# Optimization experiments

Measured on AMD Instinct MI355X. Metric: run time of the kernel, lower is better.

Reference implementation:

```python
import jax, jax.numpy as jnp
import numpy as np

EPS = 1e-7  # keras_backend.epsilon()
ROUTINGS = 3


def setup_inputs() -> dict:
    key = jax.random.key(0)
    k1, k2, k3, k4, k5 = jax.random.split(key, 5)
    B, H, W, I, O = 32, 8, 8, 32, 64
    return {
        "inputs_poses": jax.random.normal(k1, (B, H, W, I, 4, 4), dtype=jnp.float32),
        "inputs_activations": jax.random.uniform(k2, (B, H, W, I), dtype=jnp.float32),
        "w": jax.random.normal(k3, (I, O, 4, 4), dtype=jnp.float32),
        "beta_v": jax.random.normal(k4, (1, O), dtype=jnp.float32),
        "beta_a": jax.random.normal(k5, (1, O), dtype=jnp.float32),
    }


def _em_routing(votes, i_act, beta_v, beta_a, routings):
    # votes: [B, N, O, 16], i_act: [B, N]
    B, N, O, P = votes.shape
    act = i_act[..., None, None]              # [B, N, 1, 1]
    bv = beta_v[..., None, :, None]           # [1, 1, O, 1]
    ba = beta_a[..., None, :, None]           # [1, 1, O, 1]
    rr = jnp.full((N, O, 1), 1.0 / O, dtype=votes.dtype)
    it_min, it_max = 1.0, min(routings, 3.0)
    o_mean = o_act = None
    for it in range(routings):
        inv_temp = it_min + (it_max - it_min) * it / max(1.0, routings - 1.0)
        # ---- m-step ----
        rr_prime = rr * act                                    # [B, N, O, 1]
        rps = rr_prime.sum(axis=-3, keepdims=True)             # [B, 1, O, 1]
        o_mean = (rr_prime * votes).sum(axis=-3, keepdims=True) / rps   # [B,1,O,16]
        o_stdv = jnp.sqrt((rr_prime * jnp.square(votes - o_mean)).sum(axis=-3, keepdims=True) / rps)
        o_cost_h = (bv + jnp.log(o_stdv + EPS)) * rps          # [B,1,O,16]
        o_cost = o_cost_h.sum(axis=-1, keepdims=True)          # [B,1,O,1]
        o_cost_mean = o_cost.mean(axis=-2, keepdims=True)      # [B,1,1,1]
        o_cost_stdv = jnp.sqrt(jnp.square(o_cost - o_cost_mean).sum(axis=-2, keepdims=True) / O)
        o_act = jax.nn.sigmoid(inv_temp * (ba + (o_cost_mean - o_cost) / (o_cost_stdv + EPS)))
        # ---- e-step ----
        if it < routings - 1:
            o_p = (-jnp.sum(jnp.square(votes - o_mean) / (2.0 * jnp.square(o_stdv)), axis=-1, keepdims=True)
                   - jnp.sum(jnp.log(o_stdv + EPS), axis=-1, keepdims=True))   # [B,N,O,1]
            zz = jnp.log(o_act + EPS) + o_p
            rr = jax.nn.softmax(zz, axis=-2)                   # softmax over O
    poses = jnp.squeeze(o_mean, axis=-3)                       # [B, O, 16]
    activations = jnp.squeeze(o_act, axis=(-3, -1))            # [B, O]
    return poses, activations


def reference(inputs_poses, inputs_activations, w, beta_v, beta_a):
    B, H, W, I = inputs_activations.shape
    O = w.shape[1]
    # mat_transform: per-(input-type, class) 4x4 pose transform -> votes
    pose = inputs_poses.reshape(B * H * W, I, 4, 4)
    votes = jnp.einsum('siab,iobc->sioac', pose, w)            # [BHW, I, O, 4, 4]
    votes = votes.reshape(B, H, W, I, O, 16)
    # coord_addition: add scaled spatial coords to components 0 (h) and 1 (w)
    ch = jnp.zeros((1, H, 1, 1, 1, 16), votes.dtype).at[..., 0].set(
        ((jnp.arange(H, dtype=votes.dtype) + 0.5) / H).reshape(1, H, 1, 1, 1))
    cw = jnp.zeros((1, 1, W, 1, 1, 16), votes.dtype).at[..., 1].set(
        ((jnp.arange(W, dtype=votes.dtype) + 0.5) / W).reshape(1, 1, W, 1, 1))
    votes = votes + ch + cw
    votes = votes.reshape(B, H * W * I, O, 16)
    i_act = inputs_activations.reshape(B, H * W * I)
    poses, activations = _em_routing(votes, i_act, beta_v, beta_a, ROUTINGS)
    poses = poses.reshape(B, O, 4, 4)
    return poses, activations
```

## Files before the change

kernel.cpp:

```cpp
#include <hip/hip_runtime.h>


#define NB 32
#define NN 2048
#define NO 64
#define NP 16
#define EPSF 1e-7f

#define SITES_PB 8
#define IS_PB 16

#define ACC_SLOTS 33
#define ACC_PER_B (ACC_SLOTS * NO)
#define ACC_TOTAL (NB * ACC_PER_B)

template <bool FIRST>
__global__ __launch_bounds__(1024, 1) void accum_kernel(
    const float* __restrict__ pose,
    const float* __restrict__ act,
    const float* __restrict__ wmat,
    const float* __restrict__ beta_v,
    const float* __restrict__ beta_a,
    const float* __restrict__ accum_prev,
    float* __restrict__ accum_out,
    float inv_temp)
{
    __shared__ float stats_s[ACC_PER_B];
    __shared__ float buf[4][ACC_PER_B];

    const int b = blockIdx.y;
    const int sg = blockIdx.x >> 1;
    const int ig = blockIdx.x & 1;
    const int s0 = sg * SITES_PB;
    const int tid = threadIdx.x;
    const int w = tid >> 6;
    const int o = tid & 63;
    const int i = ig * 16 + w;
    const int grp = w >> 2, wvin = w & 3;

    const float4* wp = (const float4*)(wmat + ((size_t)i * 64 + o) * 16);
    float4 w0 = wp[0], w1 = wp[1], w2 = wp[2], w3 = wp[3];

    if (!FIRST && tid < 64) {
        const float* ap = accum_prev + (size_t)b * ACC_PER_B;
        float rps = ap[32 * 64 + o];
        float rinv = 1.0f / rps;
        float logsum = 0.f;
        float mm[16], vv[16];
        #pragma unroll
        for (int p = 0; p < 16; p++) {
            float mv = ap[p * 64 + o] * rinv;
            float va = fmaxf(ap[(16 + p) * 64 + o] * rinv - mv * mv, 0.f);
            mm[p] = mv;
            vv[p] = va;
            logsum += __logf(sqrtf(va) + EPSF);
        }
        float cost = rps * (16.0f * beta_v[o] + logsum);
        float cm = cost;
        #pragma unroll
        for (int s = 32; s > 0; s >>= 1) cm += __shfl_xor(cm, s, 64);
        cm *= (1.0f / 64.0f);
        float dd = cost - cm;
        float cs = dd * dd;
        #pragma unroll
        for (int s = 32; s > 0; s >>= 1) cs += __shfl_xor(cs, s, 64);
        cs = sqrtf(cs * (1.0f / 64.0f));
        float x = inv_temp * (beta_a[o] + (cm - cost) / (cs + EPSF));
        float oa = 1.0f / (1.0f + __expf(-x));
        float zzb = __logf(oa + EPSF) - logsum;
        float K = zzb;
        #pragma unroll
        for (int s = 32; s > 0; s >>= 1) K = fmaxf(K, __shfl_xor(K, s, 64));
        #pragma unroll
        for (int p = 0; p < 16; p++) stats_s[p * 64 + o] = mm[p];
        #pragma unroll
        for (int p = 0; p < 16; p++) stats_s[(16 + p) * 64 + o] = 0.5f / vv[p];
        stats_s[32 * 64 + o] = zzb - K;
    }
    __syncthreads();

    float m[16], i2v[16], zzbK = 0.f;
    if (!FIRST) {
        #pragma unroll
        for (int p = 0; p < 16; p++) m[p] = stats_s[p * 64 + o];
        #pragma unroll
        for (int p = 0; p < 16; p++) i2v[p] = stats_s[(16 + p) * 64 + o];
        zzbK = stats_s[32 * 64 + o];
    }

    float accR = 0.f, acc1[16], acc2[16];
    #pragma unroll
    for (int p = 0; p < 16; p++) { acc1[p] = 0.f; acc2[p] = 0.f; }

    const int base_n = __builtin_amdgcn_readfirstlane(s0 * 32 + ig * 16 + w);
    const float* pose_b = pose + (size_t)b * NN * 16;
    const float* act_b  = act + (size_t)b * NN;

    for (int sl = 0; sl < 8; sl++) {
        const int site = s0 + sl;
        const float c0 = ((site >> 3) + 0.5f) * 0.125f;
        const float c1 = ((site & 7) + 0.5f) * 0.125f;
        const int n = base_n + sl * 32;
        const float4* pr4 = (const float4*)(pose_b + (size_t)n * 16);
        const float av = act_b[n];

        float v[16];
        #pragma unroll
        for (int a = 0; a < 4; a++) {
            float4 pa = pr4[a];
            v[a * 4 + 0] = pa.x * w0.x + pa.y * w1.x + pa.z * w2.x + pa.w * w3.x;
            v[a * 4 + 1] = pa.x * w0.y + pa.y * w1.y + pa.z * w2.y + pa.w * w3.y;
            v[a * 4 + 2] = pa.x * w0.z + pa.y * w1.z + pa.z * w2.z + pa.w * w3.z;
            v[a * 4 + 3] = pa.x * w0.w + pa.y * w1.w + pa.z * w2.w + pa.w * w3.w;
        }
        v[0] += c0;
        v[1] += c1;

        float rr;
        if (FIRST) {
            rr = 1.0f / 64.0f;
        } else {
            float d = zzbK;
            #pragma unroll
            for (int p = 0; p < 16; p++) {
                float t = v[p] - m[p];
                d -= t * t * i2v[p];
            }
            float e = __expf(d);
            float sum = e;
            #pragma unroll
            for (int s = 32; s > 0; s >>= 1) sum += __shfl_xor(sum, s, 64);
            rr = e / fmaxf(sum, 1e-30f);
        }
        float rp = rr * av;
        accR += rp;
        #pragma unroll
        for (int p = 0; p < 16; p++) {
            acc1[p] += rp * v[p];
            acc2[p] += rp * v[p] * v[p];
        }
    }

    if (wvin == 3) {
        float* r = buf[grp];
        r[32 * 64 + o] = accR;
        #pragma unroll
        for (int p = 0; p < 16; p++) r[p * 64 + o] = acc1[p];
        #pragma unroll
        for (int p = 0; p < 16; p++) r[(16 + p) * 64 + o] = acc2[p];
    }
    __syncthreads();
    if (wvin == 2) {
        float* r = buf[grp];
        r[32 * 64 + o] += accR;
        #pragma unroll
        for (int p = 0; p < 16; p++) r[p * 64 + o] += acc1[p];
        #pragma unroll
        for (int p = 0; p < 16; p++) r[(16 + p) * 64 + o] += acc2[p];
    }
    __syncthreads();
    if (wvin == 1) {
        float* r = buf[grp];
        r[32 * 64 + o] += accR;
        #pragma unroll
        for (int p = 0; p < 16; p++) r[p * 64 + o] += acc1[p];
        #pragma unroll
        for (int p = 0; p < 16; p++) r[(16 + p) * 64 + o] += acc2[p];
    }
    __syncthreads();
    if (wvin == 0) {
        float* r = buf[grp];
        r[32 * 64 + o] += accR;
        #pragma unroll
        for (int p = 0; p < 16; p++) r[p * 64 + o] += acc1[p];
        #pragma unroll
        for (int p = 0; p < 16; p++) r[(16 + p) * 64 + o] += acc2[p];
    }
    __syncthreads();

    float* ac = accum_out + (size_t)b * ACC_PER_B;
    for (int j = tid; j < ACC_PER_B; j += 1024)
        atomicAdd(ac + j, buf[0][j] + buf[1][j] + buf[2][j] + buf[3][j]);
}

__global__ __launch_bounds__(64) void stats_final(
    const float* __restrict__ accum,
    const float* __restrict__ beta_v,
    const float* __restrict__ beta_a,
    float* __restrict__ out,
    float inv_temp)
{
    const int b = blockIdx.x;
    const int o = threadIdx.x;
    const float* ac = accum + (size_t)b * ACC_PER_B;

    float rps = ac[32 * 64 + o];
    float rinv = 1.0f / rps;
    float m[16];
    float logsum = 0.f;
    #pragma unroll
    for (int p = 0; p < 16; p++) {
        float mm = ac[p * 64 + o] * rinv;
        float vv = fmaxf(ac[(16 + p) * 64 + o] * rinv - mm * mm, 0.f);
        m[p] = mm;
        logsum += __logf(sqrtf(vv) + EPSF);
    }
    float cost = rps * (16.0f * beta_v[o] + logsum);

    float cm = cost;
    #pragma unroll
    for (int s = 32; s > 0; s >>= 1) cm += __shfl_xor(cm, s, 64);
    cm *= (1.0f / 64.0f);
    float dd = cost - cm;
    float cs = dd * dd;
    #pragma unroll
    for (int s = 32; s > 0; s >>= 1) cs += __shfl_xor(cs, s, 64);
    cs = sqrtf(cs * (1.0f / 64.0f));

    float x = inv_temp * (beta_a[o] + (cm - cost) / (cs + EPSF));
    float oa = 1.0f / (1.0f + __expf(-x));

    float* op = out + ((size_t)b * 64 + o) * 16;
    #pragma unroll
    for (int p = 0; p < 16; p++) op[p] = m[p];
    out[(size_t)NB * NO * NP + (size_t)b * 64 + o] = oa;
}

extern "C" void kernel_launch(void* const* d_in, const int* in_sizes, int n_in,
                              void* d_out, int out_size, void* d_ws, size_t ws_size,
                              hipStream_t stream) {
    const float* pose   = (const float*)d_in[0];
    const float* act    = (const float*)d_in[1];
    const float* wmat   = (const float*)d_in[2];
    const float* beta_v = (const float*)d_in[3];
    const float* beta_a = (const float*)d_in[4];
    float* out = (float*)d_out;
    float* ws = (float*)d_ws;

    float* a0 = ws;
    float* a1 = ws + (size_t)ACC_TOTAL;
    float* a2 = ws + 2 * (size_t)ACC_TOTAL;

    hipMemsetAsync(ws, 0, 3 * (size_t)ACC_TOTAL * sizeof(float), stream);

    dim3 grid(16, NB);
    accum_kernel<true ><<<grid, 1024, 0, stream>>>(pose, act, wmat, beta_v, beta_a,
                                                   nullptr, a0, 0.0f);
    accum_kernel<false><<<grid, 1024, 0, stream>>>(pose, act, wmat, beta_v, beta_a,
                                                   a0, a1, 1.0f);
    accum_kernel<false><<<grid, 1024, 0, stream>>>(pose, act, wmat, beta_v, beta_a,
                                                   a1, a2, 2.0f);
    stats_final<<<NB, 64, 0, stream>>>(a2, beta_v, beta_a, out, 3.0f);
}
```

Baseline: 146.5 us.

## Shrink accum blocks to four waves with longer site loops and register-level reduction

Each accumulation block now uses 256 threads covering 4 input types over 32 spatial sites, instead of 1024 threads covering 16 input types over 8 sites. The grid stays the same size, so each thread runs four times as many loop iterations. The cross-wave reduction becomes a two-level tree kept in registers, using half the shared buffer. Global atomics are issued straight from one wave's registers. This cuts reduction barriers, shared-memory traffic and prologue cost per unit of work, but leaves far fewer resident waves per CU, so memory and exp latency are harder to hide.

```diff
diff --git a/kernel.cpp b/kernel.cpp
--- a/kernel.cpp
+++ b/kernel.cpp
@@ -7,15 +7,12 @@
 #define NP 16
 #define EPSF 1e-7f
 
-#define SITES_PB 8
-#define IS_PB 16
-
 #define ACC_SLOTS 33
 #define ACC_PER_B (ACC_SLOTS * NO)
 #define ACC_TOTAL (NB * ACC_PER_B)
 
 template <bool FIRST>
-__global__ __launch_bounds__(1024, 1) void accum_kernel(
+__global__ __launch_bounds__(256, 2) void accum_kernel(
     const float* __restrict__ pose,
     const float* __restrict__ act,
     const float* __restrict__ wmat,
@@ -26,17 +23,16 @@
     float inv_temp)
 {
     __shared__ float stats_s[ACC_PER_B];
-    __shared__ float buf[4][ACC_PER_B];
+    __shared__ float red[2][ACC_PER_B];
 
     const int b = blockIdx.y;
-    const int sg = blockIdx.x >> 1;
-    const int ig = blockIdx.x & 1;
-    const int s0 = sg * SITES_PB;
+    const int sg = blockIdx.x >> 3;
+    const int ig = blockIdx.x & 7;
+    const int s0 = sg * 32;
     const int tid = threadIdx.x;
     const int w = tid >> 6;
     const int o = tid & 63;
-    const int i = ig * 16 + w;
-    const int grp = w >> 2, wvin = w & 3;
+    const int i = ig * 4 + w;
 
     const float4* wp = (const float4*)(wmat + ((size_t)i * 64 + o) * 16);
     float4 w0 = wp[0], w1 = wp[1], w2 = wp[2], w3 = wp[3];
@@ -92,11 +88,11 @@
     #pragma unroll
     for (int p = 0; p < 16; p++) { acc1[p] = 0.f; acc2[p] = 0.f; }
 
-    const int base_n = __builtin_amdgcn_readfirstlane(s0 * 32 + ig * 16 + w);
+    const int base_n = __builtin_amdgcn_readfirstlane(s0 * 32 + i);
     const float* pose_b = pose + (size_t)b * NN * 16;
     const float* act_b  = act + (size_t)b * NN;
 
-    for (int sl = 0; sl < 8; sl++) {
+    for (int sl = 0; sl < 32; sl++) {
         const int site = s0 + sl;
         const float c0 = ((site >> 3) + 0.5f) * 0.125f;
         const float c1 = ((site & 7) + 0.5f) * 0.125f;
@@ -141,8 +137,8 @@
         }
     }
 
-    if (wvin == 3) {
-        float* r = buf[grp];
+    if (w >= 2) {
+        float* r = red[w - 2];
         r[32 * 64 + o] = accR;
         #pragma unroll
         for (int p = 0; p < 16; p++) r[p * 64 + o] = acc1[p];
@@ -150,37 +146,39 @@
         for (int p = 0; p < 16; p++) r[(16 + p) * 64 + o] = acc2[p];
     }
     __syncthreads();
-    if (wvin == 2) {
-        float* r = buf[grp];
-        r[32 * 64 + o] += accR;
-        #pragma unroll
-        for (int p = 0; p < 16; p++) r[p * 64 + o] += acc1[p];
-        #pragma unroll
-        for (int p = 0; p < 16; p++) r[(16 + p) * 64 + o] += acc2[p];
-    }
-    __syncthreads();
-    if (wvin == 1) {
-        float* r = buf[grp];
-        r[32 * 64 + o] += accR;
-        #pragma unroll
-        for (int p = 0; p < 16; p++) r[p * 64 + o] += acc1[p];
-        #pragma unroll
-        for (int p = 0; p < 16; p++) r[(16 + p) * 64 + o] += acc2[p];
-    }
-    __syncthreads();
-    if (wvin == 0) {
-        float* r = buf[grp];
-        r[32 * 64 + o] += accR;
-        #pragma unroll
-        for (int p = 0; p < 16; p++) r[p * 64 + o] += acc1[p];
-        #pragma unroll
-        for (int p = 0; p < 16; p++) r[(16 + p) * 64 + o] += acc2[p];
-    }
-    __syncthreads();
-
-    float* ac = accum_out + (size_t)b * ACC_PER_B;
-    for (int j = tid; j < ACC_PER_B; j += 1024)
-        atomicAdd(ac + j, buf[0][j] + buf[1][j] + buf[2][j] + buf[3][j]);
+    if (w < 2) {
+        const float* r = red[w];
+        accR += r[32 * 64 + o];
+        #pragma unroll
+        for (int p = 0; p < 16; p++) acc1[p] += r[p * 64 + o];
+        #pragma unroll
+        for (int p = 0; p < 16; p++) acc2[p] += r[(16 + p) * 64 + o];
+    }
+    __syncthreads();
+    if (w == 1) {
+        float* r = red[0];
+        r[32 * 64 + o] = accR;
+        #pragma unroll
+        for (int p = 0; p < 16; p++) r[p * 64 + o] = acc1[p];
+        #pragma unroll
+        for (int p = 0; p < 16; p++) r[(16 + p) * 64 + o] = acc2[p];
+    }
+    __syncthreads();
+    if (w == 0) {
+        const float* r = red[0];
+        accR += r[32 * 64 + o];
+        #pragma unroll
+        for (int p = 0; p < 16; p++) acc1[p] += r[p * 64 + o];
+        #pragma unroll
+        for (int p = 0; p < 16; p++) acc2[p] += r[(16 + p) * 64 + o];
+
+        float* ac = accum_out + (size_t)b * ACC_PER_B;
+        atomicAdd(ac + 32 * 64 + o, accR);
+        #pragma unroll
+        for (int p = 0; p < 16; p++) atomicAdd(ac + p * 64 + o, acc1[p]);
+        #pragma unroll
+        for (int p = 0; p < 16; p++) atomicAdd(ac + (16 + p) * 64 + o, acc2[p]);
+    }
 }
 
 __global__ __launch_bounds__(64) void stats_final(
@@ -244,11 +242,11 @@
     hipMemsetAsync(ws, 0, 3 * (size_t)ACC_TOTAL * sizeof(float), stream);
 
     dim3 grid(16, NB);
-    accum_kernel<true ><<<grid, 1024, 0, stream>>>(pose, act, wmat, beta_v, beta_a,
-                                                   nullptr, a0, 0.0f);
-    accum_kernel<false><<<grid, 1024, 0, stream>>>(pose, act, wmat, beta_v, beta_a,
-                                                   a0, a1, 1.0f);
-    accum_kernel<false><<<grid, 1024, 0, stream>>>(pose, act, wmat, beta_v, beta_a,
-                                                   a1, a2, 2.0f);
+    accum_kernel<true ><<<grid, 256, 0, stream>>>(pose, act, wmat, beta_v, beta_a,
+                                                  nullptr, a0, 0.0f);
+    accum_kernel<false><<<grid, 256, 0, stream>>>(pose, act, wmat, beta_v, beta_a,
+                                                  a0, a1, 1.0f);
+    accum_kernel<false><<<grid, 256, 0, stream>>>(pose, act, wmat, beta_v, beta_a,
+                                                  a1, a2, 2.0f);
     stats_final<<<NB, 64, 0, stream>>>(a2, beta_v, beta_a, out, 3.0f);
 }
```

Result: faster. 139.8 us (-4.6%).
